# Optimization experiments

Hardware: AMD Instinct MI355X
Metric: run time of the kernel (lower is better)

The kernel has to match this reference:

```python
import jax, jax.numpy as jnp
from jax import lax
import numpy as np

ANCHOR_LENGTHS = (2.0, 4.0, 6.0, 9.0, 13.0, 18.0)  # A = 6


def make_anchors_1d(Lf, anchor_lengths):
    # anchors on the feature axis: [Lf*A, 2] (start, end)
    al = jnp.asarray(anchor_lengths, dtype=jnp.float32)          # [A]
    centers = jnp.arange(Lf, dtype=jnp.float32) + 0.5            # [Lf]
    start = centers[:, None] - 0.5 * al[None, :]                 # [Lf, A]
    end = centers[:, None] + 0.5 * al[None, :]                   # [Lf, A]
    return jnp.stack([start, end], axis=-1).reshape(Lf * al.shape[0], 2)


def setup_inputs() -> dict:
    key = jax.random.key(0)
    ks = jax.random.split(key, 4)
    B, C, Lf, A = 4, 512, 8192, len(ANCHOR_LENGTHS)
    feat = jax.random.normal(ks[0], (B, C, Lf), dtype=jnp.float32)
    conv_w = jax.random.normal(ks[1], (C, C, 3), dtype=jnp.float32) * 0.02   # OIW
    conv_b = jnp.zeros((C,), dtype=jnp.float32)
    obj_w = jax.random.normal(ks[2], (A, C, 1), dtype=jnp.float32) * 0.02
    obj_b = jnp.zeros((A,), dtype=jnp.float32)
    reg_w = jax.random.normal(ks[3], (A * 2, C, 1), dtype=jnp.float32) * 0.02
    reg_b = jnp.zeros((A * 2,), dtype=jnp.float32)
    return {"feat": feat, "conv_w": conv_w, "conv_b": conv_b,
            "obj_w": obj_w, "obj_b": obj_b, "reg_w": reg_w, "reg_b": reg_b}


def reference(feat, conv_w, conv_b, obj_w, obj_b, reg_w, reg_b):
    B, C, Lf = feat.shape
    A = obj_w.shape[0]
    # 3x1 conv, padding=1 -> SAME; layout N C W / O I W
    h = lax.conv_general_dilated(feat, conv_w, window_strides=(1,),
                                 padding="SAME",
                                 dimension_numbers=("NCH", "OIH", "NCH"))
    h = jax.nn.relu(h + conv_b[None, :, None])                   # [B, C, Lf]
    # 1x1 conv heads expressed as channel contractions
    obj = jnp.einsum("bcl,ac->bal", h, obj_w[:, :, 0]) + obj_b[None, :, None]   # [B, A, Lf]
    reg = jnp.einsum("bcl,ac->bal", h, reg_w[:, :, 0]) + reg_b[None, :, None]   # [B, 2A, Lf]
    obj = obj.transpose(0, 2, 1).reshape(B, Lf * A)                              # [B, N]
    reg = reg.transpose(0, 2, 1).reshape(B, Lf, A, 2).reshape(B, Lf * A, 2)      # [B, N, 2]
    anchors = make_anchors_1d(Lf, ANCHOR_LENGTHS)                                # [N, 2]
    return obj, reg, anchors
```

## Files before the change

### kernel.cpp

```cpp
#include <hip/hip_runtime.h>
#include <stdint.h>

typedef __attribute__((ext_vector_type(8))) short short8;
typedef __attribute__((ext_vector_type(4))) float f32x4;
typedef __attribute__((ext_vector_type(4))) float float4v;
typedef __attribute__((ext_vector_type(2))) unsigned short u16x2;
typedef __attribute__((ext_vector_type(4))) unsigned short u16x4;
typedef __attribute__((ext_vector_type(8))) unsigned short u16x8;

#define AS1 __attribute__((address_space(1)))
#define AS3 __attribute__((address_space(3)))


__device__ __forceinline__ unsigned short f2bf(float f) {
    union { float f; unsigned int u; } v; v.f = f;
    unsigned int r = v.u + 0x7fffu + ((v.u >> 16) & 1u);
    return (unsigned short)(r >> 16);
}

__constant__ float c_AL[6] = {2.f, 4.f, 6.f, 9.f, 13.f, 18.f};

__global__ __launch_bounds__(256) void prep_transpose_kernel(
    const float* __restrict__ feat, const float* __restrict__ conv_w,
    const float* __restrict__ obj_w, const float* __restrict__ reg_w,
    const float* __restrict__ obj_b, const float* __restrict__ reg_b,
    unsigned short* __restrict__ wAf, unsigned short* __restrict__ hwp,
    unsigned short* __restrict__ featT, float* __restrict__ out) {
    __shared__ unsigned short tile[64][66];
    unsigned int bx = blockIdx.x;
    int tid = threadIdx.x;
    if (bx < 4096u) {
        int l0 = (bx & 127) * 64, c0 = ((bx >> 7) & 7) * 64, b = bx >> 10;
        const float* fb = feat + ((size_t)b * 512 + c0) * 8192 + l0;
        #pragma unroll
        for (int it = 0; it < 4; ++it) {
            int slot = it * 256 + tid;
            int c = slot >> 4, l4 = (slot & 15) << 2;
            float4v v = *(const float4v*)(fb + (size_t)c * 8192 + l4);
            u16x2 p0, p1;
            p0.x = f2bf(v.x); p0.y = f2bf(v.y);
            p1.x = f2bf(v.z); p1.y = f2bf(v.w);
            *(u16x2*)(&tile[c][l4])     = p0;
            *(u16x2*)(&tile[c][l4 + 2]) = p1;
        }
        __syncthreads();
        unsigned short* ftb = featT + ((size_t)b * 8208 + 1 + l0) * 512 + c0;
        int c8 = tid & 7, lp = tid >> 3;
        unsigned int w[8];
        #pragma unroll
        for (int j = 0; j < 8; ++j)
            w[j] = *(const unsigned int*)(&tile[c8 * 8 + j][lp * 2]);
        u16x8 lo, hi;
        #pragma unroll
        for (int d = 0; d < 4; ++d) {
            unsigned int a = w[2 * d], bb = w[2 * d + 1];
            ((unsigned int*)&lo)[d] = (a & 0xffffu) | (bb << 16);
            ((unsigned int*)&hi)[d] = (a >> 16) | (bb & 0xffff0000u);
        }
        *(u16x8*)(ftb + (size_t)(lp * 2) * 512 + c8 * 8)     = lo;
        *(u16x8*)(ftb + (size_t)(lp * 2 + 1) * 512 + c8 * 8) = hi;
        return;
    }
    unsigned int idx = (bx - 4096u) * 256 + tid;
    if (idx < 786432u) {
        unsigned int chunkid = idx >> 9;
        unsigned int within = idx & 511u;
        unsigned int lane = within >> 3, j = within & 7u;
        unsigned int kc = chunkid & 15u;
        unsigned int ct = chunkid >> 4;
        unsigned int t = ct % 3u, cb = ct / 3u;
        unsigned int cout = cb * 16u + (lane & 15u);
        unsigned int cin = kc * 32u + (lane >> 4) * 8u + j;
        wAf[idx] = f2bf(conv_w[(cout * 512u + cin) * 3u + t]);
    } else if (idx < 802816u) {
        unsigned int i2 = idx - 786432u;
        unsigned int j = i2 >> 9, c = i2 & 511u;
        float v = 0.f;
        if (j < 6u) v = obj_w[j * 512u + c];
        else if (j < 18u) v = reg_w[(j - 6u) * 512u + c];
        hwp[i2] = f2bf(v);
    } else if (idx < 851968u) {
        unsigned int n = idx - 802816u;
        unsigned int l = n / 6u, a = n - l * 6u;
        float ctr = (float)l + 0.5f, half = 0.5f * c_AL[a];
        float* anchors = out + 589824;
        anchors[2 * n]     = ctr - half;
        anchors[2 * n + 1] = ctr + half;
    } else if (idx < 856064u) {
        unsigned int i4 = idx - 851968u;
        unsigned int b = i4 >> 10, rem = i4 & 1023u;
        unsigned int row = (rem >> 9) ? 8193u : 0u;
        unsigned int c = rem & 511u;
        featT[((size_t)b * 8208 + row) * 512 + c] = 0;
    } else if (idx < 1052672u) {
        unsigned int i5 = idx - 856064u;
        out[i5] = obj_b[i5 % 6u];
    } else {
        unsigned int i6 = idx - 1052672u;
        out[196608u + i6] = reg_b[i6 % 12u];
    }
}

__global__ __launch_bounds__(256, 4) void conv_gemm_kernel(
    const unsigned short* __restrict__ wAf,
    const unsigned short* __restrict__ featT,
    const float* __restrict__ conv_b,
    const unsigned short* __restrict__ hwp,
    float* __restrict__ out) {
    __shared__ unsigned short smem[17408];

    const int tid = threadIdx.x;
    const int wave = tid >> 6, lane = tid & 63;
    const int lq = lane >> 4, lr = lane & 15;
    const int l0 = blockIdx.x * 128;
    const int m0 = blockIdx.y * 128;
    const int b = blockIdx.z;
    const int wm = wave >> 1, wn = wave & 1;
    const unsigned short* ftb = featT + (size_t)b * 8208 * 512;

    f32x4 acc[4][4];
    #pragma unroll
    for (int i = 0; i < 4; ++i)
        #pragma unroll
        for (int j = 0; j < 4; ++j)
            acc[i][j] = (f32x4){0.f, 0.f, 0.f, 0.f};

    for (int kc = 0; kc < 16; ++kc) {
        __syncthreads();
        for (int ci = wave; ci < 33; ci += 4) {
            const unsigned short* g;
            if (ci < 24) {
                int t = ci >> 3, rb = ci & 7;
                g = wAf + ((size_t)(((m0 >> 4) + rb) * 3 + t) * 16 + kc) * 512 + lane * 8;
            } else {
                int lb = ci - 24;
                g = ftb + (size_t)(l0 + lb * 16 + lr) * 512 + kc * 32 + lq * 8;
            }
            __builtin_amdgcn_global_load_lds((const AS1 void*)g,
                                             (AS3 void*)(smem + ci * 512), 16, 0, 0);
        }
        __syncthreads();
        #pragma unroll
        for (int t = 0; t < 3; ++t) {
            short8 af[4], bf[4];
            #pragma unroll
            for (int fm = 0; fm < 4; ++fm)
                af[fm] = *(const short8*)(smem + ((t * 8 + wm * 4 + fm) << 9) + (lane << 3));
            #pragma unroll
            for (int fn = 0; fn < 4; ++fn) {
                int R = wn * 64 + fn * 16 + lr + t;
                bf[fn] = *(const short8*)(smem + ((24 + (R >> 4)) << 9) +
                                          ((((lq << 4) | (R & 15))) << 3));
            }
            #pragma unroll
            for (int fm = 0; fm < 4; ++fm)
                #pragma unroll
                for (int fn = 0; fn < 4; ++fn)
                    acc[fm][fn] = __builtin_amdgcn_mfma_f32_16x16x32_bf16(
                        af[fm], bf[fn], acc[fm][fn], 0, 0, 0);
        }
    }
    __syncthreads();
    #pragma unroll
    for (int fm = 0; fm < 4; ++fm) {
        int mb = wm * 64 + fm * 16 + lq * 4;
        float cb0 = conv_b[m0 + mb];
        float cb1 = conv_b[m0 + mb + 1];
        float cb2 = conv_b[m0 + mb + 2];
        float cb3 = conv_b[m0 + mb + 3];
        #pragma unroll
        for (int fn = 0; fn < 4; ++fn) {
            int n = wn * 64 + fn * 16 + lr;
            f32x4 v = acc[fm][fn];
            u16x4 pk;
            pk.x = f2bf(fmaxf(v.x + cb0, 0.f));
            pk.y = f2bf(fmaxf(v.y + cb1, 0.f));
            pk.z = f2bf(fmaxf(v.z + cb2, 0.f));
            pk.w = f2bf(fmaxf(v.w + cb3, 0.f));
            *(u16x4*)(smem + n * 136 + mb) = pk;
        }
    }
    __syncthreads();
    f32x4 hacc[2][2];
    #pragma unroll
    for (int i = 0; i < 2; ++i) {
        hacc[i][0] = (f32x4){0.f, 0.f, 0.f, 0.f};
        hacc[i][1] = (f32x4){0.f, 0.f, 0.f, 0.f};
    }
    const int lbase = wave * 32;
    for (int kk = 0; kk < 4; ++kk) {
        short8 ha[2], hb2[2];
        #pragma unroll
        for (int fm2 = 0; fm2 < 2; ++fm2)
            ha[fm2] = *(const short8*)(smem + (lbase + fm2 * 16 + lr) * 136 + kk * 32 + lq * 8);
        #pragma unroll
        for (int fn = 0; fn < 2; ++fn)
            hb2[fn] = *(const short8*)(hwp + (size_t)(fn * 16 + lr) * 512 + m0 + kk * 32 + lq * 8);
        #pragma unroll
        for (int fm2 = 0; fm2 < 2; ++fm2)
            #pragma unroll
            for (int fn = 0; fn < 2; ++fn)
                hacc[fm2][fn] = __builtin_amdgcn_mfma_f32_16x16x32_bf16(
                    ha[fm2], hb2[fn], hacc[fm2][fn], 0, 0, 0);
    }
    float* ob = out + (size_t)b * 49152;
    float* rg = out + 196608 + (size_t)b * 98304;
    #pragma unroll
    for (int fn = 0; fn < 2; ++fn) {
        int j = fn * 16 + lr;
        if (j >= 18) continue;
        #pragma unroll
        for (int fm2 = 0; fm2 < 2; ++fm2)
            #pragma unroll
            for (int r = 0; r < 4; ++r) {
                int l = l0 + lbase + fm2 * 16 + lq * 4 + r;
                float v = hacc[fm2][fn][r];
                if (j < 6) atomicAdd(ob + (size_t)l * 6 + j, v);
                else       atomicAdd(rg + (size_t)l * 12 + (j - 6), v);
            }
    }
}

extern "C" void kernel_launch(void* const* d_in, const int* in_sizes, int n_in,
                              void* d_out, int out_size, void* d_ws, size_t ws_size,
                              hipStream_t stream) {
    const float* feat   = (const float*)d_in[0];
    const float* conv_w = (const float*)d_in[1];
    const float* conv_b = (const float*)d_in[2];
    const float* obj_w  = (const float*)d_in[3];
    const float* obj_b  = (const float*)d_in[4];
    const float* reg_w  = (const float*)d_in[5];
    const float* reg_b  = (const float*)d_in[6];
    float* out = (float*)d_out;
    char* ws = (char*)d_ws;
    unsigned short* wAf   = (unsigned short*)(ws);
    unsigned short* hwp   = (unsigned short*)(ws + 1572864);
    unsigned short* featT = (unsigned short*)(ws + 1605632);

    prep_transpose_kernel<<<dim3(9744), dim3(256), 0, stream>>>(
        feat, conv_w, obj_w, reg_w, obj_b, reg_b, wAf, hwp, featT, out);
    conv_gemm_kernel<<<dim3(64, 4, 4), dim3(256), 0, stream>>>(
        wAf, featT, conv_b, hwp, out);
}
```

Before: 173.9 us.

## Replace head atomics with partial buffers and a separate reduce kernel

Each conv GEMM block used to atomically add its head partial sums into the output. It now writes them to a per-M-block partial buffer, and a new reduce kernel sums the four partials and adds the biases. The prep kernel also packs four weight conversions per thread and no longer does the bias initialisation. This removes atomic contention and the output pre-fill, at the cost of an extra kernel launch and an extra round trip through the partial buffer.

```diff
diff --git a/kernel.cpp b/kernel.cpp
--- a/kernel.cpp
+++ b/kernel.cpp
@@ -23,7 +23,6 @@
 __global__ __launch_bounds__(256) void prep_transpose_kernel(
     const float* __restrict__ feat, const float* __restrict__ conv_w,
     const float* __restrict__ obj_w, const float* __restrict__ reg_w,
-    const float* __restrict__ obj_b, const float* __restrict__ reg_b,
     unsigned short* __restrict__ wAf, unsigned short* __restrict__ hwp,
     unsigned short* __restrict__ featT, float* __restrict__ out) {
     __shared__ unsigned short tile[64][66];
@@ -62,42 +61,43 @@
         return;
     }
     unsigned int idx = (bx - 4096u) * 256 + tid;
-    if (idx < 786432u) {
-        unsigned int chunkid = idx >> 9;
-        unsigned int within = idx & 511u;
-        unsigned int lane = within >> 3, j = within & 7u;
+    if (idx < 196608u) {
+        unsigned int base = idx * 4u;
+        unsigned int chunkid = base >> 9;
+        unsigned int within = base & 511u;
+        unsigned int lane = within >> 3, j0 = within & 7u;
         unsigned int kc = chunkid & 15u;
         unsigned int ct = chunkid >> 4;
         unsigned int t = ct % 3u, cb = ct / 3u;
         unsigned int cout = cb * 16u + (lane & 15u);
-        unsigned int cin = kc * 32u + (lane >> 4) * 8u + j;
-        wAf[idx] = f2bf(conv_w[(cout * 512u + cin) * 3u + t]);
-    } else if (idx < 802816u) {
-        unsigned int i2 = idx - 786432u;
+        unsigned int cin0 = kc * 32u + (lane >> 4) * 8u + j0;
+        const float* src = conv_w + (size_t)(cout * 512u + cin0) * 3u + t;
+        u16x4 pk;
+        pk.x = f2bf(src[0]);
+        pk.y = f2bf(src[3]);
+        pk.z = f2bf(src[6]);
+        pk.w = f2bf(src[9]);
+        *(u16x4*)(wAf + base) = pk;
+    } else if (idx < 212992u) {
+        unsigned int i2 = idx - 196608u;
         unsigned int j = i2 >> 9, c = i2 & 511u;
         float v = 0.f;
         if (j < 6u) v = obj_w[j * 512u + c];
         else if (j < 18u) v = reg_w[(j - 6u) * 512u + c];
         hwp[i2] = f2bf(v);
-    } else if (idx < 851968u) {
-        unsigned int n = idx - 802816u;
+    } else if (idx < 262144u) {
+        unsigned int n = idx - 212992u;
         unsigned int l = n / 6u, a = n - l * 6u;
         float ctr = (float)l + 0.5f, half = 0.5f * c_AL[a];
         float* anchors = out + 589824;
         anchors[2 * n]     = ctr - half;
         anchors[2 * n + 1] = ctr + half;
-    } else if (idx < 856064u) {
-        unsigned int i4 = idx - 851968u;
+    } else if (idx < 266240u) {
+        unsigned int i4 = idx - 262144u;
         unsigned int b = i4 >> 10, rem = i4 & 1023u;
         unsigned int row = (rem >> 9) ? 8193u : 0u;
         unsigned int c = rem & 511u;
         featT[((size_t)b * 8208 + row) * 512 + c] = 0;
-    } else if (idx < 1052672u) {
-        unsigned int i5 = idx - 856064u;
-        out[i5] = obj_b[i5 % 6u];
-    } else {
-        unsigned int i6 = idx - 1052672u;
-        out[196608u + i6] = reg_b[i6 % 12u];
     }
 }
 
@@ -106,7 +106,7 @@
     const unsigned short* __restrict__ featT,
     const float* __restrict__ conv_b,
     const unsigned short* __restrict__ hwp,
-    float* __restrict__ out) {
+    float* __restrict__ part) {
     __shared__ unsigned short smem[17408];
 
     const int tid = threadIdx.x;
@@ -203,8 +203,7 @@
                 hacc[fm2][fn] = __builtin_amdgcn_mfma_f32_16x16x32_bf16(
                     ha[fm2], hb2[fn], hacc[fm2][fn], 0, 0, 0);
     }
-    float* ob = out + (size_t)b * 49152;
-    float* rg = out + 196608 + (size_t)b * 98304;
+    float* pb = part + ((size_t)(blockIdx.y * 4 + b) * 8192) * 18;
     #pragma unroll
     for (int fn = 0; fn < 2; ++fn) {
         int j = fn * 16 + lr;
@@ -214,11 +213,31 @@
             #pragma unroll
             for (int r = 0; r < 4; ++r) {
                 int l = l0 + lbase + fm2 * 16 + lq * 4 + r;
-                float v = hacc[fm2][fn][r];
-                if (j < 6) atomicAdd(ob + (size_t)l * 6 + j, v);
-                else       atomicAdd(rg + (size_t)l * 12 + (j - 6), v);
+                pb[(size_t)l * 18 + j] = hacc[fm2][fn][r];
             }
     }
+}
+
+__global__ __launch_bounds__(256) void reduce_kernel(
+    const float* __restrict__ part, const float* __restrict__ obj_b,
+    const float* __restrict__ reg_b, float* __restrict__ out) {
+    unsigned int idx = blockIdx.x * 256 + threadIdx.x;
+    unsigned int l = idx & 8191u, b = idx >> 13;
+    float s[18];
+    #pragma unroll
+    for (int j = 0; j < 18; ++j) s[j] = 0.f;
+    #pragma unroll
+    for (int mb = 0; mb < 4; ++mb) {
+        const float* p = part + ((size_t)(mb * 4 + b) * 8192 + l) * 18;
+        #pragma unroll
+        for (int j = 0; j < 18; ++j) s[j] += p[j];
+    }
+    float* ob = out + (size_t)b * 49152 + (size_t)l * 6;
+    #pragma unroll
+    for (int j = 0; j < 6; ++j) ob[j] = s[j] + obj_b[j];
+    float* rg = out + 196608 + (size_t)b * 98304 + (size_t)l * 12;
+    #pragma unroll
+    for (int j = 0; j < 12; ++j) rg[j] = s[6 + j] + reg_b[j];
 }
 
 extern "C" void kernel_launch(void* const* d_in, const int* in_sizes, int n_in,
@@ -236,9 +255,10 @@
     unsigned short* wAf   = (unsigned short*)(ws);
     unsigned short* hwp   = (unsigned short*)(ws + 1572864);
     unsigned short* featT = (unsigned short*)(ws + 1605632);
-
-    prep_transpose_kernel<<<dim3(9744), dim3(256), 0, stream>>>(
-        feat, conv_w, obj_w, reg_w, obj_b, reg_b, wAf, hwp, featT, out);
-    conv_gemm_kernel<<<dim3(64, 4, 4), dim3(256), 0, stream>>>(
-        wAf, featT, conv_b, hwp, out);
-}
+    float* part           = (float*)(ws + 35225600);
+
+    prep_transpose_kernel<<<dim3(5136), dim3(256), 0, stream>>>(
+        feat, conv_w, obj_w, reg_w, wAf, hwp, featT, out);
+    conv_gemm_kernel<<<dim3(64, 4, 4), dim3(256), 0, stream>>>(wAf, featT, conv_b, hwp, part);
+    reduce_kernel<<<dim3(128), dim3(256), 0, stream>>>(part, obj_b, reg_b, out);
+}
```

Result: faster. 164.1 us (median of 2 runs) (-5.6%).
